# Kernel optimization log

Hardware: AMD Instinct MI355X
Metric: run time of the kernel (lower is better)

Reference implementation:

```python
import jax, jax.numpy as jnp
import numpy as np
from jax import lax

B, T, E, H, L, V = 64, 512, 512, 1024, 2, 32000  # batch, seq, d_emb, d_hid, n_layer, n_vocab


def setup_inputs() -> dict:
    key = jax.random.key(0)
    ks = jax.random.split(key, 8)
    s = 0.03  # small init keeps tanh recurrence well-conditioned
    return {
        "src": jax.random.randint(ks[0], (B, T), 0, V),
        "emb_table": jax.random.normal(ks[1], (V, E), jnp.float32) * s,
        "W1": jax.random.normal(ks[2], (H, E), jnp.float32) * s,
        "b1": jnp.zeros((H,), jnp.float32),
        "W2": jax.random.normal(ks[3], (H, H), jnp.float32) * s,
        "b2": jnp.zeros((H,), jnp.float32),
        # layer 0 input dim = H; layers >0 input dim = 2H (bidirectional concat)
        "W_ih0": jax.random.normal(ks[4], (2, H, H), jnp.float32) * s,
        "W_ihL": jax.random.normal(ks[5], (L - 1, 2, H, 2 * H), jnp.float32) * s,
        "W_hh": jax.random.normal(ks[6], (L, 2, H, H), jnp.float32) * s,
        "b_ih": jnp.zeros((L, 2, H), jnp.float32),
        "b_hh": jnp.zeros((L, 2, H), jnp.float32),
    }


def _rnn_dir(x, Wih, Whh, bih, bhh, reverse):
    # x: [B, T, Din]. Precompute input projection as one big GEMM, then scan.
    pre = jnp.einsum('bti,hi->tbh', x, Wih) + bih  # [T, B, H]

    def step(h, p):
        h = jnp.tanh(p + h @ Whh.T + bhh)
        return h, h

    h0 = jnp.zeros((x.shape[0], Whh.shape[0]), x.dtype)
    hT, hs = lax.scan(step, h0, pre, reverse=reverse)
    return hT, jnp.transpose(hs, (1, 0, 2))  # final state [B,H], outputs [B,T,H]


def reference(src, emb_table, W1, b1, W2, b2, W_ih0, W_ihL, W_hh, b_ih, b_hh):
    # Embedding with padding_idx=0 (row zeroed)
    table = emb_table.at[0].set(0.0)
    x = table[src]  # [B, T, E]
    # emb_to_hid MLP (dropout is identity in eval mode)
    x = jax.nn.relu(x @ W1.T + b1)
    x = jax.nn.relu(x @ W2.T + b2)  # [B, T, H]
    finals = []
    inp = x
    for l in range(L):
        Wih = W_ih0 if l == 0 else W_ihL[l - 1]
        hf, of = _rnn_dir(inp, Wih[0], W_hh[l, 0], b_ih[l, 0], b_hh[l, 0], False)
        hb, ob = _rnn_dir(inp, Wih[1], W_hh[l, 1], b_ih[l, 1], b_hh[l, 1], True)
        finals += [hf, hb]
        inp = jnp.concatenate([of, ob], axis=-1)  # [B, T, 2H]
    # torch h_n layout: [n_layer * num_directions, B, H], layer-major, dir-minor
    return jnp.stack(finals, axis=0)
```

## Files before the change

### kernel.cpp

```cpp
#include <hip/hip_runtime.h>


typedef _Float16 f16;
typedef _Float16 f16x8 __attribute__((ext_vector_type(8)));
typedef _Float16 f16x4 __attribute__((ext_vector_type(4)));
typedef float f32x4 __attribute__((ext_vector_type(4)));

static const size_t MB_ = 1024ull * 1024ull;
static const size_t OFF_X0    = 0;
static const size_t OFF_X1    = 64 * MB_;
static const size_t OFF_EMB   = OFF_X1;
static const size_t OFF_MLP1  = 96 * MB_;
static const size_t OFF_H     = 192 * MB_;
static const size_t OFF_FLAGS = 192 * MB_ + 512 * 1024;
static const size_t OFF_BIAS  = 192 * MB_ + 576 * 1024;
static const size_t OFF_W1C   = 193 * MB_;
static const size_t OFF_W2C   = 194 * MB_;
static const size_t WS_NEED   = 196 * MB_;

__device__ __forceinline__ void gld16(const void* g, void* l) {
#if __has_builtin(__builtin_amdgcn_global_load_lds)
  __builtin_amdgcn_global_load_lds((const __attribute__((address_space(1))) void*)g,
                                   (__attribute__((address_space(3))) void*)l, 16, 0, 0);
#else
  *(f16x8*)l = *(const f16x8*)g;
#endif
}

__device__ __forceinline__ float tanh_fast(float x) {
  float ax = __builtin_fabsf(x);
  float e = __builtin_amdgcn_exp2f(ax * 2.8853900817779268f);
  float r = 1.0f - 2.0f * __builtin_amdgcn_rcpf(e + 1.0f);
  return __builtin_copysignf(r, x);
}


__global__ void zero_k(unsigned int* __restrict__ p, int n) {
  int i = blockIdx.x * blockDim.x + threadIdx.x;
  if (i < n) p[i] = 0u;
}

__global__ void cvt_k(const float* __restrict__ in, f16* __restrict__ out, int n4) {
  int i = blockIdx.x * blockDim.x + threadIdx.x;
  int stride = gridDim.x * blockDim.x;
  for (; i < n4; i += stride) {
    float4 v = ((const float4*)in)[i];
    f16x4 o = {(f16)v.x, (f16)v.y, (f16)v.z, (f16)v.w};
    ((f16x4*)out)[i] = o;
  }
}

__global__ void bias_k(const float* __restrict__ a, const float* __restrict__ b, float* __restrict__ o) {
  int i = blockIdx.x * blockDim.x + threadIdx.x;
  if (i < 4096) o[i] = a[i] + b[i];
}

__global__ void embed_k(const int* __restrict__ src, const float* __restrict__ tab, f16* __restrict__ out) {
  int m = blockIdx.x;
  int tid = threadIdx.x;
  int tok = src[m];
  f16x4 o = {(f16)0.f, (f16)0.f, (f16)0.f, (f16)0.f};
  if (tok != 0) {
    float4 v = *(const float4*)(tab + (size_t)tok * 512 + tid * 4);
    o[0] = (f16)v.x; o[1] = (f16)v.y; o[2] = (f16)v.z; o[3] = (f16)v.w;
  }
  *(f16x4*)(out + (size_t)m * 512 + tid * 4) = o;
}

template <int EPI>
__global__ __launch_bounds__(256) void gemm_f16(
    const f16* __restrict__ A, int lda, const f16* __restrict__ Bw,
    f16* __restrict__ out, const float* __restrict__ bias, int M, int N, int K) {
  __shared__ alignas(16) f16 As[4096];
  __shared__ alignas(16) f16 Bs[4096];
  const int nt = N >> 7;
  const int bx = blockIdx.x;
  const int tm = bx / nt, tn = bx - tm * nt;
  const int tid = threadIdx.x;
  const int l = tid & 63, w = tid >> 6;
  const int wr = w >> 1, wc = w & 1;
  const int srow = (w << 4) + (l >> 2);
  const int scol = (l & 3) << 3;
  const f16* Ab = A + (size_t)(tm * 128 + srow) * lda + scol;
  const f16* Bb = Bw + (size_t)(tn * 128 + srow) * K + scol;
  f32x4 acc[4][4];
#pragma unroll
  for (int i = 0; i < 4; i++)
#pragma unroll
    for (int j = 0; j < 4; j++) acc[i][j] = (f32x4){0.f, 0.f, 0.f, 0.f};
  const int ar = l & 15, ak = (l >> 4) << 3;
  for (int k0 = 0; k0 < K; k0 += 32) {
    gld16(Ab + k0, &As[tid * 8]);
    gld16(Ab + (size_t)64 * lda + k0, &As[tid * 8 + 2048]);
    gld16(Bb + k0, &Bs[tid * 8]);
    gld16(Bb + (size_t)64 * K + k0, &Bs[tid * 8 + 2048]);
    __syncthreads();
    f16x8 av[4], bv[4];
#pragma unroll
    for (int i = 0; i < 4; i++) av[i] = *(const f16x8*)&As[(wr * 64 + i * 16 + ar) * 32 + ak];
#pragma unroll
    for (int j = 0; j < 4; j++) bv[j] = *(const f16x8*)&Bs[(wc * 64 + j * 16 + ar) * 32 + ak];
#pragma unroll
    for (int i = 0; i < 4; i++)
#pragma unroll
      for (int j = 0; j < 4; j++)
        acc[i][j] = __builtin_amdgcn_mfma_f32_16x16x32_f16(av[i], bv[j], acc[i][j], 0, 0, 0);
    __syncthreads();
  }
  const int r0 = (l >> 4) << 2, c0 = l & 15;
#pragma unroll
  for (int i = 0; i < 4; i++) {
#pragma unroll
    for (int j = 0; j < 4; j++) {
      const int col = tn * 128 + wc * 64 + j * 16 + c0;
      const float bc = (EPI & 1) ? bias[col] : 0.f;
#pragma unroll
      for (int r = 0; r < 4; r++) {
        const int row = tm * 128 + wr * 64 + i * 16 + r0 + r;
        float v = acc[i][j][r];
        if (EPI & 1) { v += bc; v = v > 0.f ? v : 0.f; }
        if (EPI & 2) {
          const int b_ = row >> 9, t = row & 511;
          out[((size_t)(t * 64 + b_) << 10) + col] = (f16)v;
        } else {
          out[(size_t)row * N + col] = (f16)v;
        }
      }
    }
  }
}

template <int LAYER>
__global__ __launch_bounds__(512, 1) void rnn_scan(
    const f16* __restrict__ X,
    const float* __restrict__ Wih,
    const float* __restrict__ Whh,
    const float* __restrict__ bsum,
    f16* __restrict__ hbuf,
    unsigned int* __restrict__ flags,
    f16* __restrict__ seqout,
    float* __restrict__ dout) {
  constexpr int KX = LAYER ? 2048 : 1024;
  constexpr int XSH = LAYER ? 11 : 10;
  constexpr int NKX = KX / 128;
  constexpr int NKH = 8;
  const int bid = blockIdx.x;
  const int dir = bid >> 7, bg = (bid >> 6) & 1, cg = bid & 63;
  const int tid = threadIdx.x, l = tid & 63, w = tid >> 6;
  const int mi = w & 1, kq = w >> 1;
  __shared__ alignas(16) f16 Wl[16 * 1024];
  __shared__ alignas(16) f16 Wi[16 * KX];
  __shared__ f32x4 part[2][4][64];
  __shared__ alignas(16) f16 p2[32][16];
  __shared__ unsigned int cnt;
  const int ld = LAYER * 2 + dir;
  if (tid == 0) cnt = 0u;
  for (int ch = tid; ch < 2048; ch += 512) {
    const int n = ch >> 7, k0 = (ch & 127) << 3;
    const float* wp = Whh + (((size_t)(ld * 1024 + cg * 16 + n)) << 10) + k0;
    float4 v0 = *(const float4*)wp, v1 = *(const float4*)(wp + 4);
    f16x8 hv = {(f16)v0.x, (f16)v0.y, (f16)v0.z, (f16)v0.w,
                (f16)v1.x, (f16)v1.y, (f16)v1.z, (f16)v1.w};
    *(f16x8*)&Wl[(n << 10) + (k0 ^ ((n & 7) << 3))] = hv;
  }
  for (int ch = tid; ch < (16 * KX / 8); ch += 512) {
    const int n = ch >> (XSH - 3), k0 = (ch & (KX / 8 - 1)) << 3;
    const float* wp = Wih + ((size_t)(dir * 1024 + cg * 16 + n)) * KX + k0;
    float4 v0 = *(const float4*)wp, v1 = *(const float4*)(wp + 4);
    f16x8 hv = {(f16)v0.x, (f16)v0.y, (f16)v0.z, (f16)v0.w,
                (f16)v1.x, (f16)v1.y, (f16)v1.z, (f16)v1.w};
    *(f16x8*)&Wi[(n << XSH) + (k0 ^ ((n & 7) << 3))] = hv;
  }
  const float bn = bsum[(ld << 10) + cg * 16 + (l & 15)];
  f16* hD = hbuf + ((size_t)dir << 17);
  unsigned int* fl = flags + ((dir * 2 + bg) << 10);
  const int arow = bg * 32 + mi * 16 + (l & 15);
  const int akh = (kq << 8) + ((l >> 4) << 3);
  const int akx = kq * (KX / 4) + ((l >> 4) << 3);
  const int wn = l & 15;
  const int wsw = (wn & 7) << 3;

  f16x8 xv[NKX];
  {
    const int t0 = dir ? 511 : 0;
    const f16* xr = X + (((size_t)(t0 * 64 + arow)) << XSH) + akx;
#pragma unroll
    for (int i = 0; i < NKX; i++)
      asm volatile("global_load_dwordx4 %0, %1, off offset:%2"
                   : "=&v"(xv[i]) : "v"(xr), "i"(64 * i));
  }
  __syncthreads();

  for (int s = 0; s < 512; ++s) {
    const int t = dir ? (511 - s) : s;
    f32x4 acc = {0.f, 0.f, 0.f, 0.f};
    if (s > 0) {
      if (w == 7) {
        const unsigned int tgt = (unsigned int)(LAYER * 512 + s);
        unsigned int* fp = fl + l * 16;
        for (;;) {
          unsigned int f = __hip_atomic_load(fp, __ATOMIC_RELAXED, __HIP_MEMORY_SCOPE_AGENT);
          if (__all((int)(f >= tgt))) break;
        }
      }
      __syncthreads();
      const f16* hrow = hD + (((size_t)(s & 1)) << 16) + (((size_t)arow) << 10) + akh;
      f16x8 hv[NKH];
#pragma unroll
      for (int i = 0; i < NKH; i++)
        asm volatile("global_load_dwordx4 %0, %1, off offset:%2 sc0 sc1"
                     : "=&v"(hv[i]) : "v"(hrow), "i"(64 * i));
      asm volatile("s_waitcnt vmcnt(%0)" :: "i"(NKH) : "memory");
      __builtin_amdgcn_sched_barrier(0);
#pragma unroll
      for (int it = 0; it < NKX; ++it) {
        const int ko = akx + it * 32;
        f16x8 bv = *(const f16x8*)&Wi[(wn << XSH) + (ko ^ wsw)];
        acc = __builtin_amdgcn_mfma_f32_16x16x32_f16(xv[it], bv, acc, 0, 0, 0);
      }
      asm volatile("s_waitcnt vmcnt(0)" ::: "memory");
      __builtin_amdgcn_sched_barrier(0);
#pragma unroll
      for (int it = 0; it < NKH; ++it) {
        const int ko = akh + it * 32;
        f16x8 bv = *(const f16x8*)&Wl[(wn << 10) + (ko ^ wsw)];
        acc = __builtin_amdgcn_mfma_f32_16x16x32_f16(hv[it], bv, acc, 0, 0, 0);
      }
    } else {
      asm volatile("s_waitcnt vmcnt(0)" ::: "memory");
      __builtin_amdgcn_sched_barrier(0);
#pragma unroll
      for (int it = 0; it < NKX; ++it) {
        const int ko = akx + it * 32;
        f16x8 bv = *(const f16x8*)&Wi[(wn << XSH) + (ko ^ wsw)];
        acc = __builtin_amdgcn_mfma_f32_16x16x32_f16(xv[it], bv, acc, 0, 0, 0);
      }
    }
    part[mi][kq][l] = acc;
    __syncthreads();
    if (w < 2) {
      f32x4 sum = part[w][0][l];
      sum += part[w][1][l];
      sum += part[w][2][l];
      sum += part[w][3][l];
#pragma unroll
      for (int r = 0; r < 4; ++r) {
        const int row = ((l >> 4) << 2) + r;
        float v = tanh_fast(sum[r] + bn);
        p2[(w << 4) + row][l & 15] = (f16)v;
        if (s == 511) {
          const int b_ = bg * 32 + (w << 4) + row;
          dout[(((size_t)(ld * 64 + b_)) << 10) + cg * 16 + (l & 15)] = v;
        }
      }
      asm volatile("s_waitcnt lgkmcnt(0)" ::: "memory");
      __builtin_amdgcn_sched_barrier(0);
      if (l < 32) {
        const int rr = (w << 4) + (l >> 1), hf = l & 1;
        f16x8 pv = *(const f16x8*)&p2[rr][hf * 8];
        const int b_ = bg * 32 + rr;
        f16* hp = hD + (((size_t)((s + 1) & 1)) << 16) + (((size_t)b_) << 10) + cg * 16 + hf * 8;
        asm volatile("global_store_dwordx4 %0, %1, off sc0 sc1" :: "v"(hp), "v"(pv) : "memory");
        if (LAYER == 0) {
          f16* sp = seqout + (((size_t)(t * 64 + b_)) << 11) + (dir << 10) + cg * 16 + hf * 8;
          asm volatile("global_store_dwordx4 %0, %1, off" :: "v"(sp), "v"(pv) : "memory");
        }
      }
      asm volatile("s_waitcnt vmcnt(0)" ::: "memory");
      __builtin_amdgcn_sched_barrier(0);
      if (l == 0) {
        unsigned int old = __hip_atomic_fetch_add(&cnt, 1u, __ATOMIC_RELAXED,
                                                  __HIP_MEMORY_SCOPE_WORKGROUP);
        if (old == (unsigned int)(2 * s + 1))
          __hip_atomic_store(&fl[cg * 16], (unsigned int)(LAYER * 512 + s + 1),
                             __ATOMIC_RELAXED, __HIP_MEMORY_SCOPE_AGENT);
      }
    }
    if (s + 1 < 512) {
      const int tn_ = dir ? (511 - (s + 1)) : (s + 1);
      const f16* xr = X + (((size_t)(tn_ * 64 + arow)) << XSH) + akx;
#pragma unroll
      for (int i = 0; i < NKX; i++)
        asm volatile("global_load_dwordx4 %0, %1, off offset:%2"
                     : "=&v"(xv[i]) : "v"(xr), "i"(64 * i));
    }
  }
}


extern "C" void kernel_launch(void* const* d_in, const int* in_sizes, int n_in,
                              void* d_out, int out_size, void* d_ws, size_t ws_size,
                              hipStream_t stream) {
  const int* src    = (const int*)d_in[0];
  const float* emb  = (const float*)d_in[1];
  const float* W1   = (const float*)d_in[2];
  const float* b1   = (const float*)d_in[3];
  const float* W2   = (const float*)d_in[4];
  const float* b2   = (const float*)d_in[5];
  const float* Wih0 = (const float*)d_in[6];
  const float* WihL = (const float*)d_in[7];
  const float* Whh  = (const float*)d_in[8];
  const float* bih  = (const float*)d_in[9];
  const float* bhh  = (const float*)d_in[10];
  float* out = (float*)d_out;
  char* ws = (char*)d_ws;

  if (ws_size < WS_NEED) {
    zero_k<<<(out_size + 255) / 256, 256, 0, stream>>>((unsigned int*)d_out, out_size);
    return;
  }

  f16* X0   = (f16*)(ws + OFF_X0);
  f16* X1   = (f16*)(ws + OFF_X1);
  f16* EMB  = (f16*)(ws + OFF_EMB);
  f16* MLP1 = (f16*)(ws + OFF_MLP1);
  f16* HB   = (f16*)(ws + OFF_H);
  unsigned int* FLAGS = (unsigned int*)(ws + OFF_FLAGS);
  float* BIAS = (float*)(ws + OFF_BIAS);
  f16* W1C  = (f16*)(ws + OFF_W1C);
  f16* W2C  = (f16*)(ws + OFF_W2C);

  cvt_k<<<256, 256, 0, stream>>>(W1, W1C, 131072);
  cvt_k<<<256, 256, 0, stream>>>(W2, W2C, 262144);
  bias_k<<<16, 256, 0, stream>>>(bih, bhh, BIAS);
  zero_k<<<16, 256, 0, stream>>>(FLAGS, 4096);

  embed_k<<<32768, 128, 0, stream>>>(src, emb, EMB);
  gemm_f16<1><<<2048, 256, 0, stream>>>(EMB, 512, W1C, MLP1, b1, 32768, 1024, 512);
  gemm_f16<3><<<2048, 256, 0, stream>>>(MLP1, 1024, W2C, X0, b2, 32768, 1024, 1024);

  rnn_scan<0><<<256, 512, 0, stream>>>(X0, Wih0, Whh, BIAS, HB, FLAGS, X1, out);
  rnn_scan<1><<<256, 512, 0, stream>>>(X1, WihL, Whh, BIAS, HB, FLAGS, nullptr, out);
}
```

Baseline: 5.902 ms.

## Precompute RNN input projections with full GEMMs before the recurrent scan

```diff
diff --git a/kernel.cpp b/kernel.cpp
--- a/kernel.cpp
+++ b/kernel.cpp
@@ -17,6 +17,19 @@
 static const size_t OFF_W1C   = 193 * MB_;
 static const size_t OFF_W2C   = 194 * MB_;
 static const size_t WS_NEED   = 196 * MB_;
+static const size_t P_X0    = 0;
+static const size_t P_X1    = 0;
+static const size_t P_PRE   = 128 * MB_;
+static const size_t P_EMB   = 128 * MB_;
+static const size_t P_MLP1  = 160 * MB_;
+static const size_t P_H     = 256 * MB_;
+static const size_t P_FLAGS = 256 * MB_ + 512 * 1024;
+static const size_t P_BIAS  = 256 * MB_ + 576 * 1024;
+static const size_t P_W1C   = 257 * MB_;
+static const size_t P_W2C   = 258 * MB_;
+static const size_t P_WIH0C = 260 * MB_;
+static const size_t P_WIHLC = 264 * MB_;
+static const size_t WS_NEED2 = 272 * MB_;
 
 __device__ __forceinline__ void gld16(const void* g, void* l) {
 #if __has_builtin(__builtin_amdgcn_global_load_lds)
@@ -132,14 +145,9 @@
 
 template <int LAYER>
 __global__ __launch_bounds__(512, 1) void rnn_scan(
-    const f16* __restrict__ X,
-    const float* __restrict__ Wih,
-    const float* __restrict__ Whh,
-    const float* __restrict__ bsum,
-    f16* __restrict__ hbuf,
-    unsigned int* __restrict__ flags,
-    f16* __restrict__ seqout,
-    float* __restrict__ dout) {
+    const f16* __restrict__ X, const float* __restrict__ Wih, const float* __restrict__ Whh,
+    const float* __restrict__ bsum, f16* __restrict__ hbuf, unsigned int* __restrict__ flags,
+    f16* __restrict__ seqout, float* __restrict__ dout) {
   constexpr int KX = LAYER ? 2048 : 1024;
   constexpr int XSH = LAYER ? 11 : 10;
   constexpr int NKX = KX / 128;
@@ -287,6 +295,132 @@
   }
 }
 
+template <int LAYER>
+__global__ __launch_bounds__(512, 1) void rnn_scan_pre(
+    const f16* __restrict__ PRE,
+    const float* __restrict__ Whh,
+    const float* __restrict__ bsum,
+    f16* __restrict__ hbuf,
+    unsigned int* __restrict__ flags,
+    f16* __restrict__ seqout,
+    float* __restrict__ dout) {
+  constexpr int NKH = 8;
+  const int bid = blockIdx.x;
+  const int dir = bid >> 7, bg = (bid >> 6) & 1, cg = bid & 63;
+  const int tid = threadIdx.x, l = tid & 63, w = tid >> 6;
+  const int mi = w & 1, kq = w >> 1;
+  __shared__ alignas(16) f16 Wl[16 * 1024];
+  __shared__ f32x4 part[2][4][64];
+  __shared__ alignas(16) f16 p2[32][16];
+  __shared__ unsigned int cnt;
+  const int ld = LAYER * 2 + dir;
+  if (tid == 0) cnt = 0u;
+  for (int ch = tid; ch < 2048; ch += 512) {
+    const int n = ch >> 7, k0 = (ch & 127) << 3;
+    const float* wp = Whh + (((size_t)(ld * 1024 + cg * 16 + n)) << 10) + k0;
+    float4 v0 = *(const float4*)wp, v1 = *(const float4*)(wp + 4);
+    f16x8 hv = {(f16)v0.x, (f16)v0.y, (f16)v0.z, (f16)v0.w,
+                (f16)v1.x, (f16)v1.y, (f16)v1.z, (f16)v1.w};
+    *(f16x8*)&Wl[(n << 10) + (k0 ^ ((n & 7) << 3))] = hv;
+  }
+  const float bn = bsum[(ld << 10) + cg * 16 + (l & 15)];
+  const f16* preD = PRE + (((size_t)dir) << 25);
+  f16* hD = hbuf + ((size_t)dir << 17);
+  unsigned int* fl = flags + ((dir * 2 + bg) << 10);
+  const int arow = bg * 32 + mi * 16 + (l & 15);
+  const int akh = (kq << 8) + ((l >> 4) << 3);
+  const int wn = l & 15;
+  const int wsw = (wn & 7) << 3;
+  const int prow = bg * 32 + (w << 4) + ((l >> 4) << 2);
+  const int pcol = cg * 16 + (l & 15);
+
+  float pv0 = 0.f, pv1 = 0.f, pv2 = 0.f, pv3 = 0.f;
+  if (w < 2) {
+    const int t0 = dir ? 511 : 0;
+    const f16* pp = preD + (((size_t)(t0 * 64 + prow)) << 10) + pcol;
+    pv0 = (float)pp[0]; pv1 = (float)pp[1 << 10];
+    pv2 = (float)pp[2 << 10]; pv3 = (float)pp[3 << 10];
+  }
+  __syncthreads();
+
+  for (int s = 0; s < 512; ++s) {
+    const int t = dir ? (511 - s) : s;
+    f32x4 acc = {0.f, 0.f, 0.f, 0.f};
+    if (s > 0) {
+      if (w == 7) {
+        const unsigned int tgt = (unsigned int)(LAYER * 512 + s);
+        unsigned int* fp = fl + l * 16;
+        for (;;) {
+          unsigned int f = __hip_atomic_load(fp, __ATOMIC_RELAXED, __HIP_MEMORY_SCOPE_AGENT);
+          if (__all((int)(f >= tgt))) break;
+        }
+      }
+      __syncthreads();
+      const f16* hrow = hD + (((size_t)(s & 1)) << 16) + (((size_t)arow) << 10) + akh;
+      f16x8 hv[NKH];
+#pragma unroll
+      for (int i = 0; i < NKH; i++)
+        asm volatile("global_load_dwordx4 %0, %1, off offset:%2 sc0 sc1"
+                     : "=&v"(hv[i]) : "v"(hrow), "i"(64 * i));
+      asm volatile("s_waitcnt vmcnt(0)" ::: "memory");
+      __builtin_amdgcn_sched_barrier(0);
+#pragma unroll
+      for (int it = 0; it < NKH; ++it) {
+        const int ko = akh + it * 32;
+        f16x8 bv = *(const f16x8*)&Wl[(wn << 10) + (ko ^ wsw)];
+        acc = __builtin_amdgcn_mfma_f32_16x16x32_f16(hv[it], bv, acc, 0, 0, 0);
+      }
+    }
+    part[mi][kq][l] = acc;
+    __syncthreads();
+    if (w < 2) {
+      f32x4 sum = part[w][0][l];
+      sum += part[w][1][l];
+      sum += part[w][2][l];
+      sum += part[w][3][l];
+      float pva[4] = {pv0, pv1, pv2, pv3};
+#pragma unroll
+      for (int r = 0; r < 4; ++r) {
+        const int row = ((l >> 4) << 2) + r;
+        float v = tanh_fast(sum[r] + pva[r] + bn);
+        p2[(w << 4) + row][l & 15] = (f16)v;
+        if (s == 511) {
+          const int b_ = bg * 32 + (w << 4) + row;
+          dout[(((size_t)(ld * 64 + b_)) << 10) + cg * 16 + (l & 15)] = v;
+        }
+      }
+      asm volatile("s_waitcnt lgkmcnt(0)" ::: "memory");
+      __builtin_amdgcn_sched_barrier(0);
+      if (l < 32) {
+        const int rr = (w << 4) + (l >> 1), hf = l & 1;
+        f16x8 pv = *(const f16x8*)&p2[rr][hf * 8];
+        const int b_ = bg * 32 + rr;
+        f16* hp = hD + (((size_t)((s + 1) & 1)) << 16) + (((size_t)b_) << 10) + cg * 16 + hf * 8;
+        asm volatile("global_store_dwordx4 %0, %1, off sc0 sc1" :: "v"(hp), "v"(pv) : "memory");
+        if (LAYER == 0) {
+          f16* sp = seqout + (((size_t)(t * 64 + b_)) << 11) + (dir << 10) + cg * 16 + hf * 8;
+          asm volatile("global_store_dwordx4 %0, %1, off" :: "v"(sp), "v"(pv) : "memory");
+        }
+      }
+      asm volatile("s_waitcnt vmcnt(0)" ::: "memory");
+      __builtin_amdgcn_sched_barrier(0);
+      if (l == 0) {
+        unsigned int old = __hip_atomic_fetch_add(&cnt, 1u, __ATOMIC_RELAXED,
+                                                  __HIP_MEMORY_SCOPE_WORKGROUP);
+        if (old == (unsigned int)(2 * s + 1))
+          __hip_atomic_store(&fl[cg * 16], (unsigned int)(LAYER * 512 + s + 1),
+                             __ATOMIC_RELAXED, __HIP_MEMORY_SCOPE_AGENT);
+      }
+      if (s + 1 < 512) {
+        const int tn_ = dir ? (511 - (s + 1)) : (s + 1);
+        const f16* pp = preD + (((size_t)(tn_ * 64 + prow)) << 10) + pcol;
+        pv0 = (float)pp[0]; pv1 = (float)pp[1 << 10];
+        pv2 = (float)pp[2 << 10]; pv3 = (float)pp[3 << 10];
+      }
+    }
+  }
+}
+
 
 extern "C" void kernel_launch(void* const* d_in, const int* in_sizes, int n_in,
                               void* d_out, int out_size, void* d_ws, size_t ws_size,
@@ -305,6 +439,43 @@
   float* out = (float*)d_out;
   char* ws = (char*)d_ws;
 
+  if (ws_size >= WS_NEED2) {
+    f16* X0   = (f16*)(ws + P_X0);
+    f16* X1   = (f16*)(ws + P_X1);
+    f16* PRE  = (f16*)(ws + P_PRE);
+    f16* EMB  = (f16*)(ws + P_EMB);
+    f16* MLP1 = (f16*)(ws + P_MLP1);
+    f16* HB   = (f16*)(ws + P_H);
+    unsigned int* FLAGS = (unsigned int*)(ws + P_FLAGS);
+    float* BIAS = (float*)(ws + P_BIAS);
+    f16* W1C  = (f16*)(ws + P_W1C);
+    f16* W2C  = (f16*)(ws + P_W2C);
+    f16* WIH0C = (f16*)(ws + P_WIH0C);
+    f16* WIHLC = (f16*)(ws + P_WIHLC);
+
+    cvt_k<<<256, 256, 0, stream>>>(W1, W1C, 131072);
+    cvt_k<<<256, 256, 0, stream>>>(W2, W2C, 262144);
+    cvt_k<<<512, 256, 0, stream>>>(Wih0, WIH0C, 524288);
+    cvt_k<<<512, 256, 0, stream>>>(WihL, WIHLC, 1048576);
+    bias_k<<<16, 256, 0, stream>>>(bih, bhh, BIAS);
+    zero_k<<<16, 256, 0, stream>>>(FLAGS, 4096);
+
+    embed_k<<<32768, 128, 0, stream>>>(src, emb, EMB);
+    gemm_f16<1><<<2048, 256, 0, stream>>>(EMB, 512, W1C, MLP1, b1, 32768, 1024, 512);
+    gemm_f16<3><<<2048, 256, 0, stream>>>(MLP1, 1024, W2C, X0, b2, 32768, 1024, 1024);
+
+    gemm_f16<0><<<2048, 256, 0, stream>>>(X0, 1024, WIH0C, PRE, nullptr, 32768, 1024, 1024);
+    gemm_f16<0><<<2048, 256, 0, stream>>>(X0, 1024, WIH0C + (1u << 20), PRE + (1ull << 25),
+                                          nullptr, 32768, 1024, 1024);
+    rnn_scan_pre<0><<<256, 512, 0, stream>>>(PRE, Whh, BIAS, HB, FLAGS, X1, out);
+
+    gemm_f16<0><<<2048, 256, 0, stream>>>(X1, 2048, WIHLC, PRE, nullptr, 32768, 1024, 2048);
+    gemm_f16<0><<<2048, 256, 0, stream>>>(X1, 2048, WIHLC + (1u << 21), PRE + (1ull << 25),
+                                          nullptr, 32768, 1024, 2048);
+    rnn_scan_pre<1><<<256, 512, 0, stream>>>(PRE, Whh, BIAS, HB, FLAGS, nullptr, out);
+    return;
+  }
+
   if (ws_size < WS_NEED) {
     zero_k<<<(out_size + 255) / 256, 256, 0, stream>>>((unsigned int*)d_out, out_size);
     return;
```

New measurement: 5.898 ms. About the same (-0.1%).
